# Kernel tuning notes

Measured on AMD Instinct MI355X. Metric: run time of the kernel, lower is better.

The kernel has to match this reference:

```python
import jax, jax.numpy as jnp
import numpy as np

THRESHOLD = 0.5
TEMPERATURE = 4.0
LOG_CLAMP = -100.0  # torch BCELoss clamps log terms at -100

B, C, K = 131072, 128, 64


def setup_inputs() -> dict:
    key = jax.random.key(0)
    k1, k2, k3, k4, k5 = jax.random.split(key, 5)
    # sigmoid-like probabilities in (0, 1)
    output = jax.random.uniform(k1, (B, C), dtype=jnp.float32)
    output_consistency = jax.random.uniform(k2, (B, C), dtype=jnp.float32)
    label = jax.random.uniform(k3, (B, C), dtype=jnp.float32)
    class_idx = jnp.sort(jax.random.randint(k4, (K,), 0, C)).astype(jnp.int64)
    batch_mask = jax.random.randint(k5, (B,), 0, 2).astype(bool)
    return {
        "output": output,
        "output_consistency": output_consistency,
        "label": label,
        "class_idx": class_idx,
        "batch_mask": batch_mask,
    }


def _clamped_log(x):
    return jnp.maximum(jnp.log(x), LOG_CLAMP)


def reference(output, output_consistency, label, class_idx, batch_mask):
    # gather the class columns of interest: [B, K]
    o = output[:, class_idx]
    oc = output_consistency[:, class_idx]
    y = label[:, class_idx]

    # sharpened pseudo-label (branch on threshold, fused via where)
    sharp = jnp.where(o > THRESHOLD,
                      o + (1.0 - o) / TEMPERATURE,
                      o - o / TEMPERATURE)

    # per-element BCE (torch BCELoss semantics with log clamp)
    bce = -(y * _clamped_log(o) + (1.0 - y) * _clamped_log(1.0 - o))
    pseudo = (o - sharp) ** 2          # F.mse_loss on scalars
    consistency = (oc - sharp) ** 2

    per_elem = bce + pseudo + consistency            # [B, K]
    row_mask = batch_mask.astype(per_elem.dtype)     # [B]
    total = jnp.sum(per_elem * row_mask[:, None])
    cnt = jnp.sum(row_mask) * per_elem.shape[1]
    return total / cnt
```

## Files before the change

kernel.cpp:

```cpp
#include <hip/hip_runtime.h>

#define BLOCK   256
#define B_ROWS  131072
#define C_COLS  128
#define K_SEL   64
#define TOTAL_VEC (B_ROWS * C_COLS / 4)
#define NTHREADS  (TOTAL_VEC / 2)
#define GRID      (NTHREADS / BLOCK)

#define WS_PARTIALS_OFF 1024

__global__ void build_w(const int* __restrict__ class_idx,
                        float* __restrict__ w)
{
    int c = threadIdx.x;
    int cnt = 0;
    #pragma unroll
    for (int k = 0; k < K_SEL; ++k)
        cnt += (class_idx[k] == c) ? 1 : 0;
    w[c] = (float)cnt;
}

__device__ __forceinline__ float fast_log(float x) {
    return __log2f(x) * 0.6931471805599453f;
}

__device__ __forceinline__ float per_elem_loss(float o, float oc, float y,
                                               float wc) {
    float sharp = (o > 0.5f) ? (o + (1.0f - o) * 0.25f)
                             : (o - o * 0.25f);
    float lo  = fmaxf(fast_log(o),        -100.0f);
    float l1o = fmaxf(fast_log(1.0f - o), -100.0f);
    float bce = -(y * lo + (1.0f - y) * l1o);
    float dp = o  - sharp;
    float dc = oc - sharp;
    return wc * (bce + dp * dp + dc * dc);
}

__global__ __launch_bounds__(BLOCK) void semi_loss_main(
    const float* __restrict__ out,
    const float* __restrict__ outc,
    const float* __restrict__ lab,
    const int*  __restrict__ batch_mask,
    const float* __restrict__ wtab,
    float2* __restrict__ partials)
{
    const int tid = blockIdx.x * BLOCK + threadIdx.x;
    const int v0  = tid;
    const int v1  = tid + NTHREADS;
    const int c4  = v0 & 31;

    const int m0 = batch_mask[v0 >> 5];
    const int m1 = batch_mask[v1 >> 5];
    const float4 w4  = ((const float4*)wtab)[c4];

    const float4 o0  = ((const float4*)out )[v0];
    const float4 oc0 = ((const float4*)outc)[v0];
    const float4 y0  = ((const float4*)lab )[v0];
    const float4 o1  = ((const float4*)out )[v1];
    const float4 oc1 = ((const float4*)outc)[v1];
    const float4 y1  = ((const float4*)lab )[v1];

    const float mf0 = m0 ? 1.0f : 0.0f;
    const float mf1 = m1 ? 1.0f : 0.0f;

    float s0 = per_elem_loss(o0.x, oc0.x, y0.x, w4.x)
             + per_elem_loss(o0.y, oc0.y, y0.y, w4.y)
             + per_elem_loss(o0.z, oc0.z, y0.z, w4.z)
             + per_elem_loss(o0.w, oc0.w, y0.w, w4.w);
    float s1 = per_elem_loss(o1.x, oc1.x, y1.x, w4.x)
             + per_elem_loss(o1.y, oc1.y, y1.y, w4.y)
             + per_elem_loss(o1.z, oc1.z, y1.z, w4.z)
             + per_elem_loss(o1.w, oc1.w, y1.w, w4.w);

    float sum  = mf0 * s0 + mf1 * s1;
    float cntf = (c4 == 0) ? (mf0 + mf1) : 0.0f;

    #pragma unroll
    for (int off = 32; off > 0; off >>= 1) {
        sum  += __shfl_down(sum,  off);
        cntf += __shfl_down(cntf, off);
    }
    __shared__ float ssum[BLOCK / 64];
    __shared__ float scnt[BLOCK / 64];
    int wave = threadIdx.x >> 6;
    int lane = threadIdx.x & 63;
    if (lane == 0) { ssum[wave] = sum; scnt[wave] = cntf; }
    __syncthreads();
    if (threadIdx.x == 0) {
        float s = 0.0f, c = 0.0f;
        #pragma unroll
        for (int i = 0; i < BLOCK / 64; ++i) { s += ssum[i]; c += scnt[i]; }
        partials[blockIdx.x] = make_float2(s, c);
    }
}

__global__ __launch_bounds__(BLOCK) void semi_loss_reduce(
    const float2* __restrict__ partials, float* __restrict__ out)
{
    double s = 0.0, c = 0.0;
    for (int i = threadIdx.x; i < GRID; i += BLOCK) {
        float2 p = partials[i];
        s += (double)p.x;
        c += (double)p.y;
    }
    #pragma unroll
    for (int off = 32; off > 0; off >>= 1) {
        s += __shfl_down(s, off);
        c += __shfl_down(c, off);
    }
    __shared__ double dsum[BLOCK / 64];
    __shared__ double dcnt[BLOCK / 64];
    int wave = threadIdx.x >> 6;
    int lane = threadIdx.x & 63;
    if (lane == 0) { dsum[wave] = s; dcnt[wave] = c; }
    __syncthreads();
    if (threadIdx.x == 0) {
        double ts = 0.0, tc = 0.0;
        #pragma unroll
        for (int i = 0; i < BLOCK / 64; ++i) { ts += dsum[i]; tc += dcnt[i]; }
        out[0] = (float)(ts / (tc * (double)K_SEL));
    }
}

extern "C" void kernel_launch(void* const* d_in, const int* in_sizes, int n_in,
                              void* d_out, int out_size, void* d_ws, size_t ws_size,
                              hipStream_t stream) {
    const float* out_p  = (const float*)d_in[0];
    const float* outc_p = (const float*)d_in[1];
    const float* lab_p  = (const float*)d_in[2];
    const int*   cidx_p = (const int*)d_in[3];
    const int*   mask_p = (const int*)d_in[4];

    float*  wtab     = (float*)d_ws;
    float2* partials = (float2*)((char*)d_ws + WS_PARTIALS_OFF);

    build_w<<<1, C_COLS, 0, stream>>>(cidx_p, wtab);
    semi_loss_main<<<GRID, BLOCK, 0, stream>>>(out_p, outc_p, lab_p,
                                               mask_p, wtab, partials);
    semi_loss_reduce<<<1, BLOCK, 0, stream>>>(partials, (float*)d_out);
}
```

Baseline: 207.8 us.

## Process 64 rows per block and skip loads for masked-out rows

```diff
diff --git a/kernel.cpp b/kernel.cpp
--- a/kernel.cpp
+++ b/kernel.cpp
@@ -4,9 +4,10 @@
 #define B_ROWS  131072
 #define C_COLS  128
 #define K_SEL   64
-#define TOTAL_VEC (B_ROWS * C_COLS / 4)
-#define NTHREADS  (TOTAL_VEC / 2)
-#define GRID      (NTHREADS / BLOCK)
+#define ROWS_PER_BLOCK 64
+#define GRID    (B_ROWS / ROWS_PER_BLOCK)
+#define F4_PER_BLOCK (ROWS_PER_BLOCK * C_COLS / 4)
+#define ITERS   (F4_PER_BLOCK / BLOCK)
 
 #define WS_PARTIALS_OFF 1024
 
@@ -45,36 +46,39 @@
     const float* __restrict__ wtab,
     float2* __restrict__ partials)
 {
-    const int tid = blockIdx.x * BLOCK + threadIdx.x;
-    const int v0  = tid;
-    const int v1  = tid + NTHREADS;
-    const int c4  = v0 & 31;
+    __shared__ float wm[ROWS_PER_BLOCK];
 
-    const int m0 = batch_mask[v0 >> 5];
-    const int m1 = batch_mask[v1 >> 5];
-    const float4 w4  = ((const float4*)wtab)[c4];
+    const int row0 = blockIdx.x * ROWS_PER_BLOCK;
+    float cntf = 0.0f;
+    if (threadIdx.x < ROWS_PER_BLOCK) {
+        float m = batch_mask[row0 + threadIdx.x] ? 1.0f : 0.0f;
+        wm[threadIdx.x] = m;
+        cntf = m;
+    }
 
-    const float4 o0  = ((const float4*)out )[v0];
-    const float4 oc0 = ((const float4*)outc)[v0];
-    const float4 y0  = ((const float4*)lab )[v0];
-    const float4 o1  = ((const float4*)out )[v1];
-    const float4 oc1 = ((const float4*)outc)[v1];
-    const float4 y1  = ((const float4*)lab )[v1];
+    const int   c4 = threadIdx.x & 31;
+    const float4 w4 = ((const float4*)wtab)[c4];
 
-    const float mf0 = m0 ? 1.0f : 0.0f;
-    const float mf1 = m1 ? 1.0f : 0.0f;
+    __syncthreads();
 
-    float s0 = per_elem_loss(o0.x, oc0.x, y0.x, w4.x)
-             + per_elem_loss(o0.y, oc0.y, y0.y, w4.y)
-             + per_elem_loss(o0.z, oc0.z, y0.z, w4.z)
-             + per_elem_loss(o0.w, oc0.w, y0.w, w4.w);
-    float s1 = per_elem_loss(o1.x, oc1.x, y1.x, w4.x)
-             + per_elem_loss(o1.y, oc1.y, y1.y, w4.y)
-             + per_elem_loss(o1.z, oc1.z, y1.z, w4.z)
-             + per_elem_loss(o1.w, oc1.w, y1.w, w4.w);
+    const int vbase = blockIdx.x * F4_PER_BLOCK + threadIdx.x;
+    const int rsub  = threadIdx.x >> 5;
+    float sum = 0.0f;
 
-    float sum  = mf0 * s0 + mf1 * s1;
-    float cntf = (c4 == 0) ? (mf0 + mf1) : 0.0f;
+    #pragma unroll
+    for (int i = 0; i < ITERS; ++i) {
+        const float m = wm[i * 8 + rsub];
+        if (m > 0.0f) {
+            const int v = vbase + i * BLOCK;
+            float4 o4  = ((const float4*)out )[v];
+            float4 oc4 = ((const float4*)outc)[v];
+            float4 y4  = ((const float4*)lab )[v];
+            sum += per_elem_loss(o4.x, oc4.x, y4.x, w4.x)
+                 + per_elem_loss(o4.y, oc4.y, y4.y, w4.y)
+                 + per_elem_loss(o4.z, oc4.z, y4.z, w4.z)
+                 + per_elem_loss(o4.w, oc4.w, y4.w, w4.w);
+        }
+    }
 
     #pragma unroll
     for (int off = 32; off > 0; off >>= 1) {
```

Measured after the change: 186.5 us. 10.3% less time.
